# Optimization experiments

Hardware: AMD Instinct MI355X
Metric: run time of the kernel (lower is better)

The kernel has to match this reference:

```python
import jax, jax.numpy as jnp
import numpy as np

DMODEL = 512
NUM_HEADS = 8
DK = DMODEL // NUM_HEADS  # 64
CAUSAL = True


def setup_inputs() -> dict:
    key = jax.random.key(0)
    ks = jax.random.split(key, 11)
    B, S = 4, 2048
    s_in = 1.0 / np.sqrt(DMODEL)
    s_out = 1.0 / np.sqrt(NUM_HEADS * DK)
    return {
        "Q": jax.random.normal(ks[0], (B, S, DMODEL), jnp.float32),
        "K": jax.random.normal(ks[1], (B, S, DMODEL), jnp.float32),
        "V": jax.random.normal(ks[2], (B, S, DMODEL), jnp.float32),
        # torch nn.Linear weights stored as [in, out] (already transposed)
        "WQ_w": jax.random.uniform(ks[3], (DMODEL, DK), jnp.float32, -s_in, s_in),
        "WQ_b": jax.random.uniform(ks[4], (DK,), jnp.float32, -s_in, s_in),
        "WK_w": jax.random.uniform(ks[5], (DMODEL, DK), jnp.float32, -s_in, s_in),
        "WK_b": jax.random.uniform(ks[6], (DK,), jnp.float32, -s_in, s_in),
        "WV_w": jax.random.uniform(ks[7], (DMODEL, DK), jnp.float32, -s_in, s_in),
        "WV_b": jax.random.uniform(ks[8], (DK,), jnp.float32, -s_in, s_in),
        "Wo_w": jax.random.uniform(ks[9], (NUM_HEADS * DK, DMODEL), jnp.float32, -s_out, s_out),
        "Wo_b": jax.random.uniform(ks[10], (DMODEL,), jnp.float32, -s_out, s_out),
    }


def reference(Q, K, V, WQ_w, WQ_b, WK_w, WK_b, WV_w, WV_b, Wo_w, Wo_b):
    # Single shared projection to dk=64 (NOT per-head in the original module)
    q = Q @ WQ_w + WQ_b  # [B,S,dk]
    k = K @ WK_w + WK_b  # [B,S,dk]
    v = V @ WV_w + WV_b  # [B,S,dk]
    scores = jnp.einsum("bsd,btd->bst", q, k) / np.sqrt(DK).astype(np.float32)
    if CAUSAL:
        S = scores.shape[-1]
        causal = jnp.tril(jnp.ones((S, S), dtype=bool))  # True = keep
        scores = jnp.where(causal, scores, -jnp.inf)
    attn = jax.nn.softmax(scores, axis=-1)
    head_out = jnp.einsum("bst,btd->bsd", attn, v)  # [B,S,dk]
    # Every head is identical -> concat == tile num_heads copies
    concat = jnp.tile(head_out, (1, 1, NUM_HEADS))  # [B,S,num_heads*dk]
    return concat @ Wo_w + Wo_b  # [B,S,dmodel]
```

## Files before the change

### kernel.cpp

```cpp
#include <hip/hip_runtime.h>

#define DMODEL 512
#define DK 64
#define NH 8
#define SEQ 2048
#define BATCH 4
#define NROWS 8192
#define NEGBIG -1.0e30f
#define SPLITW 8
#define DKP 66
#define SHIFT2 8.656170245f
#define QSCALE 0.1803368801f

typedef _Float16 half_t;
typedef _Float16 half4 __attribute__((ext_vector_type(4)));
typedef _Float16 half8 __attribute__((ext_vector_type(8)));
typedef float floatx4 __attribute__((ext_vector_type(4)));

#ifdef __has_builtin
#  if __has_builtin(__builtin_amdgcn_exp2f)
#    define EXP2F(x) __builtin_amdgcn_exp2f(x)
#  endif
#  if __has_builtin(__builtin_amdgcn_cvt_pkrtz)
#    define HAVE_PKRTZ 1
#  endif
#  if __has_builtin(__builtin_amdgcn_mfma_f32_16x16x16f16)
#    define HAVE_MFMA16 1
#  endif
#endif
#ifndef EXP2F
#  define EXP2F(x) exp2f(x)
#endif
#ifndef HAVE_PKRTZ
#  define HAVE_PKRTZ 0
#endif
#ifndef HAVE_MFMA16
#  define HAVE_MFMA16 0
#endif

__device__ __forceinline__ half4 pk4(const float* p) {
#if HAVE_PKRTZ
    half4 r;
    auto lo = __builtin_amdgcn_cvt_pkrtz(p[0], p[1]);
    auto hi = __builtin_amdgcn_cvt_pkrtz(p[2], p[3]);
    __builtin_memcpy(&r, &lo, 4);
    __builtin_memcpy(reinterpret_cast<char*>(&r) + 4, &hi, 4);
    return r;
#else
    return (half4){(half_t)p[0], (half_t)p[1], (half_t)p[2], (half_t)p[3]};
#endif
}

__global__ __launch_bounds__(256) void prep_kernel(
    const float* __restrict__ WQ, const float* __restrict__ WK,
    const float* __restrict__ WV, const float* __restrict__ Wo,
    half_t* __restrict__ wtq, half_t* __restrict__ wtk, half_t* __restrict__ wtv,
    half_t* __restrict__ wo_tr)
{
    const int idx = blockIdx.x * 256 + threadIdx.x;
    const int k = idx >> 6;
    const int n = idx & 63;
    wtq[(size_t)n * DMODEL + k] = (half_t)WQ[idx];
    wtk[(size_t)n * DMODEL + k] = (half_t)WK[idx];
    wtv[(size_t)n * DMODEL + k] = (half_t)WV[idx];
    const int n2 = idx & 511;
    const int k2 = idx >> 9;
    float s = 0.f;
#pragma unroll
    for (int h = 0; h < NH; h++)
        s += Wo[((size_t)(h * DK + k2)) * DMODEL + n2];
    wo_tr[(size_t)n2 * DK + k2] = (half_t)s;
}

__global__ __launch_bounds__(128) void proj_kernel(
    const float* __restrict__ Q, const float* __restrict__ K, const float* __restrict__ V,
    const half_t* __restrict__ wtq, const half_t* __restrict__ wtk, const half_t* __restrict__ wtv,
    const float* __restrict__ bQ, const float* __restrict__ bK, const float* __restrict__ bV,
    half_t* __restrict__ qh, half_t* __restrict__ kh, half_t* __restrict__ vt)
{
    const int tens = blockIdx.y;
    const float* X  = (tens == 0) ? Q : (tens == 1) ? K : V;
    const half_t* wt = (tens == 0) ? wtq : (tens == 1) ? wtk : wtv;
    const float* bias = (tens == 0) ? bQ : (tens == 1) ? bK : bV;

    const int r0 = blockIdx.x * 16;
    const int tid = threadIdx.x;
    const int w = tid >> 6;
    const int lane = tid & 63;
    const int c = lane & 15;
    const int quad = lane >> 4;

    __shared__ floatx4 red[4][64];

    floatx4 acc[4] = {{0.f,0.f,0.f,0.f},{0.f,0.f,0.f,0.f},{0.f,0.f,0.f,0.f},{0.f,0.f,0.f,0.f}};

    const float* xrow = X + (size_t)(r0 + c) * DMODEL + quad * 8;
#pragma unroll 8
    for (int ks = w; ks < 16; ks += 2) {
        const float* xp = xrow + ks * 32;
        half8 a;
#pragma unroll
        for (int i = 0; i < 8; i++) a[i] = (half_t)xp[i];
#pragma unroll
        for (int nt = 0; nt < 4; nt++) {
            half8 bfr = *(const half8*)(wt + (size_t)(nt * 16 + c) * DMODEL + ks * 32 + quad * 8);
            acc[nt] = __builtin_amdgcn_mfma_f32_16x16x32_f16(a, bfr, acc[nt], 0, 0, 0);
        }
    }

    if (w == 1) {
#pragma unroll
        for (int nt = 0; nt < 4; nt++) red[nt][lane] = acc[nt];
    }
    __syncthreads();
    if (w == 1) return;

#pragma unroll
    for (int nt = 0; nt < 4; nt++) {
        const floatx4 r4 = red[nt][lane];
        const float bv = bias[nt * 16 + c];
#pragma unroll
        for (int r = 0; r < 4; r++) {
            const float val = acc[nt][r] + r4[r] + bv;
            const int row = r0 + quad * 4 + r;
            if (tens == 0) {
                qh[(size_t)row * DK + nt * 16 + c] = (half_t)(val * QSCALE);
            } else if (tens == 1) {
                kh[(size_t)row * DK + nt * 16 + c] = (half_t)val;
            } else {
                const int b  = row >> 11;
                const int s  = row & (SEQ - 1);
                const int kb = s >> 4;
                const int kk = s & 15;
                vt[(size_t)(b * 128 + kb) * 1024
                   + (size_t)c * 64 + (nt >> 1) * 32 + (kk >> 2) * 8 + (nt & 1) * 4 + (kk & 3)]
                    = (half_t)val;
            }
        }
    }
}

__global__ __launch_bounds__(512, 4) void attn_kernel(
    const half_t* __restrict__ qh, const half_t* __restrict__ kh,
    const half_t* __restrict__ vt, const half_t* __restrict__ wo_tr,
    const float* __restrict__ bo, float* __restrict__ out)
{
    const int bx = blockIdx.x;
    int b, qt;
    if (bx < 256) { qt = bx >> 1;            b = bx & 1; }
    else          { int k2 = bx - 256; qt = 127 - (k2 >> 1); b = 2 + (k2 & 1); }
    const int tid = threadIdx.x;
    const int w = tid >> 6;
    const int lane = tid & 63;
    const int c = lane & 15;
    const int quad = lane >> 4;

    __shared__ float sow[SPLITW][16][DKP];
    __shared__ float sl_s[SPLITW][16];
    __shared__ half_t of16[16][72];

    const half_t* qrow = qh + (size_t)(b * SEQ + qt * 16 + c) * DK + quad * 8;
    half8 qb0 = *(const half8*)(qrow);
    half8 qb1 = *(const half8*)(qrow + 32);

    float lp = 0.f;
    floatx4 o[4] = {{0.f,0.f,0.f,0.f},{0.f,0.f,0.f,0.f},{0.f,0.f,0.f,0.f},{0.f,0.f,0.f,0.f}};
    const floatx4 cinit = {-SHIFT2, -SHIFT2, -SHIFT2, -SHIFT2};

    const half_t* kbb = kh + (size_t)b * SEQ * DK;
    const half_t* vtb = vt + (size_t)b * 128 * 1024;

    int pb = w;
    half8 ka0, ka1, kb0, kb1;
    if (2 * pb <= qt) {
        const half_t* kr0 = kbb + (size_t)(2 * pb * 16 + c) * DK + quad * 8;
        ka0 = *(const half8*)(kr0);
        ka1 = *(const half8*)(kr0 + 32);
        const half_t* kr1 = kr0 + 16 * DK;
        kb0 = *(const half8*)(kr1);
        kb1 = *(const half8*)(kr1 + 32);
    }

    while (2 * pb <= qt) {
        const int t0 = 2 * pb, t1 = 2 * pb + 1;
        const half_t* vp0 = vtb + (size_t)t0 * 1024 + c * 64 + quad * 8;
        const half_t* vp1 = vtb + (size_t)t1 * 1024 + c * 64 + quad * 8;
        half8 va01 = *(const half8*)(vp0);
        half8 va23 = *(const half8*)(vp0 + 32);
        half8 vc01 = *(const half8*)(vp1);
        half8 vc23 = *(const half8*)(vp1 + 32);

        const int npb = pb + SPLITW;
        half8 nka0 = ka0, nka1 = ka1, nkb0 = kb0, nkb1 = kb1;
        if (2 * npb <= qt) {
            const half_t* nkr0 = kbb + (size_t)(2 * npb * 16 + c) * DK + quad * 8;
            nka0 = *(const half8*)(nkr0);
            nka1 = *(const half8*)(nkr0 + 32);
            const half_t* nkr1 = nkr0 + 16 * DK;
            nkb0 = *(const half8*)(nkr1);
            nkb1 = *(const half8*)(nkr1 + 32);
        }

        floatx4 sc0 = cinit;
        sc0 = __builtin_amdgcn_mfma_f32_16x16x32_f16(ka0, qb0, sc0, 0, 0, 0);
        sc0 = __builtin_amdgcn_mfma_f32_16x16x32_f16(ka1, qb1, sc0, 0, 0, 0);
        floatx4 sc1 = cinit;
        sc1 = __builtin_amdgcn_mfma_f32_16x16x32_f16(kb0, qb0, sc1, 0, 0, 0);
        sc1 = __builtin_amdgcn_mfma_f32_16x16x32_f16(kb1, qb1, sc1, 0, 0, 0);

        if (t0 == qt) {
#pragma unroll
            for (int r = 0; r < 4; r++) {
                if (quad * 4 + r > c) sc0[r] = NEGBIG;
                sc1[r] = NEGBIG;
            }
        } else if (t1 == qt) {
#pragma unroll
            for (int r = 0; r < 4; r++)
                if (quad * 4 + r > c) sc1[r] = NEGBIG;
        }

        float p0[4], p1[4];
#pragma unroll
        for (int r = 0; r < 4; r++) { p0[r] = EXP2F(sc0[r]); p1[r] = EXP2F(sc1[r]); }
        lp += (p0[0] + p0[1]) + (p0[2] + p0[3]) + ((p1[0] + p1[1]) + (p1[2] + p1[3]));

#if HAVE_MFMA16
        half4 pa = pk4(p0), pc = pk4(p1);
        half4 va0 = __builtin_shufflevector(va01, va01, 0, 1, 2, 3);
        half4 va1 = __builtin_shufflevector(va01, va01, 4, 5, 6, 7);
        half4 va2 = __builtin_shufflevector(va23, va23, 0, 1, 2, 3);
        half4 va3 = __builtin_shufflevector(va23, va23, 4, 5, 6, 7);
        half4 vc0 = __builtin_shufflevector(vc01, vc01, 0, 1, 2, 3);
        half4 vc1 = __builtin_shufflevector(vc01, vc01, 4, 5, 6, 7);
        half4 vc2 = __builtin_shufflevector(vc23, vc23, 0, 1, 2, 3);
        half4 vc3 = __builtin_shufflevector(vc23, vc23, 4, 5, 6, 7);
        o[0] = __builtin_amdgcn_mfma_f32_16x16x16f16(pa, va0, o[0], 0, 0, 0);
        o[1] = __builtin_amdgcn_mfma_f32_16x16x16f16(pa, va1, o[1], 0, 0, 0);
        o[2] = __builtin_amdgcn_mfma_f32_16x16x16f16(pa, va2, o[2], 0, 0, 0);
        o[3] = __builtin_amdgcn_mfma_f32_16x16x16f16(pa, va3, o[3], 0, 0, 0);
        o[0] = __builtin_amdgcn_mfma_f32_16x16x16f16(pc, vc0, o[0], 0, 0, 0);
        o[1] = __builtin_amdgcn_mfma_f32_16x16x16f16(pc, vc1, o[1], 0, 0, 0);
        o[2] = __builtin_amdgcn_mfma_f32_16x16x16f16(pc, vc2, o[2], 0, 0, 0);
        o[3] = __builtin_amdgcn_mfma_f32_16x16x16f16(pc, vc3, o[3], 0, 0, 0);
#else
        half8 pa8, pc8;
#pragma unroll
        for (int jj = 0; jj < 8; jj++) {
            const int src = (((quad * 2 + (jj >> 2)) & 3) * 16 + c);
            const float pj0 = __shfl(p0[jj & 3], src);
            const float pj1 = __shfl(p1[jj & 3], src);
            pa8[jj] = (quad < 2) ? (half_t)pj0 : (half_t)0.f;
            pc8[jj] = (quad < 2) ? (half_t)pj1 : (half_t)0.f;
        }
#pragma unroll
        for (int nt = 0; nt < 4; nt++) {
            const half_t* vb0 = vtb + (size_t)t0 * 1024 + c * 64 + (nt >> 1) * 32 + (quad & 1) * 16 + (nt & 1) * 4;
            half4 l0 = *(const half4*)(vb0);
            half4 h0 = *(const half4*)(vb0 + 8);
            half8 v80 = {l0[0], l0[1], l0[2], l0[3], h0[0], h0[1], h0[2], h0[3]};
            o[nt] = __builtin_amdgcn_mfma_f32_16x16x32_f16(pa8, v80, o[nt], 0, 0, 0);
            const half_t* vb1 = vtb + (size_t)t1 * 1024 + c * 64 + (nt >> 1) * 32 + (quad & 1) * 16 + (nt & 1) * 4;
            half4 l1 = *(const half4*)(vb1);
            half4 h1 = *(const half4*)(vb1 + 8);
            half8 v81 = {l1[0], l1[1], l1[2], l1[3], h1[0], h1[1], h1[2], h1[3]};
            o[nt] = __builtin_amdgcn_mfma_f32_16x16x32_f16(pc8, v81, o[nt], 0, 0, 0);
        }
#endif
        ka0 = nka0; ka1 = nka1; kb0 = nkb0; kb1 = nkb1; pb = npb;
    }

    lp += __shfl_xor(lp, 16);
    lp += __shfl_xor(lp, 32);

#pragma unroll
    for (int nt = 0; nt < 4; nt++)
#pragma unroll
        for (int r = 0; r < 4; r++)
            sow[w][quad * 4 + r][nt * 16 + c] = o[nt][r];
    if (quad == 0) sl_s[w][c] = lp;
    __syncthreads();

    {
        const int q = w * 2 + (lane >> 5);
        const int d0 = (lane & 31) * 2;
        float lstar = 0.f, acc0 = 0.f, acc1 = 0.f;
#pragma unroll
        for (int ww = 0; ww < SPLITW; ww++) {
            lstar += sl_s[ww][q];
            const float* sp = &sow[ww][q][d0];
            acc0 += sp[0];
            acc1 += sp[1];
        }
        const float linv = 1.f / lstar;
        of16[q][d0]     = (half_t)(acc0 * linv);
        of16[q][d0 + 1] = (half_t)(acc1 * linv);
    }
    __syncthreads();

    half8 a1 = *(const half8*)(&of16[c][quad * 8]);
    half8 a2 = *(const half8*)(&of16[c][32 + quad * 8]);
    const size_t orow = (size_t)(b * SEQ + qt * 16);
#pragma unroll
    for (int i = 0; i < 4; i++) {
        const int n = (w * 4 + i) * 16 + c;
        half8 b1 = *(const half8*)(wo_tr + (size_t)n * DK + quad * 8);
        half8 b2 = *(const half8*)(wo_tr + (size_t)n * DK + 32 + quad * 8);
        floatx4 oc = {0.f, 0.f, 0.f, 0.f};
        oc = __builtin_amdgcn_mfma_f32_16x16x32_f16(a1, b1, oc, 0, 0, 0);
        oc = __builtin_amdgcn_mfma_f32_16x16x32_f16(a2, b2, oc, 0, 0, 0);
        const float bv = bo[n];
#pragma unroll
        for (int r = 0; r < 4; r++)
            out[(orow + quad * 4 + r) * DMODEL + n] = oc[r] + bv;
    }
}

extern "C" void kernel_launch(void* const* d_in, const int* in_sizes, int n_in,
                              void* d_out, int out_size, void* d_ws, size_t ws_size,
                              hipStream_t stream) {
    const float* Q  = (const float*)d_in[0];
    const float* K  = (const float*)d_in[1];
    const float* V  = (const float*)d_in[2];
    const float* WQ = (const float*)d_in[3];
    const float* bQ = (const float*)d_in[4];
    const float* WK = (const float*)d_in[5];
    const float* bK = (const float*)d_in[6];
    const float* WV = (const float*)d_in[7];
    const float* bV = (const float*)d_in[8];
    const float* Wo = (const float*)d_in[9];
    const float* bo = (const float*)d_in[10];
    float* out = (float*)d_out;

    char* ws = (char*)d_ws;
    half_t* qh    = (half_t*)ws;
    half_t* kh    = (half_t*)(ws + (1u << 20));
    half_t* vt    = (half_t*)(ws + (2u << 20));
    half_t* wtq   = (half_t*)(ws + (3u << 20));
    half_t* wtk   = wtq + 32768;
    half_t* wtv   = wtk + 32768;
    half_t* wo_tr = wtv + 32768;

    prep_kernel<<<128, 256, 0, stream>>>(WQ, WK, WV, Wo, wtq, wtk, wtv, wo_tr);
    proj_kernel<<<dim3(512, 3), 128, 0, stream>>>(Q, K, V, wtq, wtk, wtv, bQ, bK, bV, qh, kh, vt);
    attn_kernel<<<512, 512, 0, stream>>>(qh, kh, vt, wo_tr, bo, out);
}
```

Before: 142.0 us.

## Fuse prep, projection and attention into one persistent kernel with grid barriers

Merges the three kernel launches (weight prep, QKV projection, attention plus output projection) into one 512-block kernel separated by software grid barriers built on atomic counters, with a memset to reset the counters. This removes the gaps and tail effects between launches. The barrier assumes all 512 blocks are resident at once, and it has a guard timeout that could silently break correctness if they are not. Packing three projection tiles per block into four 128-thread groups leaves one group idle during that phase.

```diff
diff --git a/kernel.cpp b/kernel.cpp
--- a/kernel.cpp
+++ b/kernel.cpp
@@ -5,7 +5,7 @@
 #define NH 8
 #define SEQ 2048
 #define BATCH 4
-#define NROWS 8192
+#define NBLOCKS 512
 #define NEGBIG -1.0e30f
 #define SPLITW 8
 #define DKP 66
@@ -51,268 +51,288 @@
 #endif
 }
 
-__global__ __launch_bounds__(256) void prep_kernel(
-    const float* __restrict__ WQ, const float* __restrict__ WK,
-    const float* __restrict__ WV, const float* __restrict__ Wo,
-    half_t* __restrict__ wtq, half_t* __restrict__ wtk, half_t* __restrict__ wtv,
-    half_t* __restrict__ wo_tr)
-{
-    const int idx = blockIdx.x * 256 + threadIdx.x;
-    const int k = idx >> 6;
-    const int n = idx & 63;
-    wtq[(size_t)n * DMODEL + k] = (half_t)WQ[idx];
-    wtk[(size_t)n * DMODEL + k] = (half_t)WK[idx];
-    wtv[(size_t)n * DMODEL + k] = (half_t)WV[idx];
-    const int n2 = idx & 511;
-    const int k2 = idx >> 9;
-    float s = 0.f;
-#pragma unroll
-    for (int h = 0; h < NH; h++)
-        s += Wo[((size_t)(h * DK + k2)) * DMODEL + n2];
-    wo_tr[(size_t)n2 * DK + k2] = (half_t)s;
-}
-
-__global__ __launch_bounds__(128) void proj_kernel(
-    const float* __restrict__ Q, const float* __restrict__ K, const float* __restrict__ V,
-    const half_t* __restrict__ wtq, const half_t* __restrict__ wtk, const half_t* __restrict__ wtv,
-    const float* __restrict__ bQ, const float* __restrict__ bK, const float* __restrict__ bV,
-    half_t* __restrict__ qh, half_t* __restrict__ kh, half_t* __restrict__ vt)
-{
-    const int tens = blockIdx.y;
-    const float* X  = (tens == 0) ? Q : (tens == 1) ? K : V;
-    const half_t* wt = (tens == 0) ? wtq : (tens == 1) ? wtk : wtv;
-    const float* bias = (tens == 0) ? bQ : (tens == 1) ? bK : bV;
-
-    const int r0 = blockIdx.x * 16;
-    const int tid = threadIdx.x;
-    const int w = tid >> 6;
-    const int lane = tid & 63;
-    const int c = lane & 15;
-    const int quad = lane >> 4;
-
-    __shared__ floatx4 red[4][64];
-
-    floatx4 acc[4] = {{0.f,0.f,0.f,0.f},{0.f,0.f,0.f,0.f},{0.f,0.f,0.f,0.f},{0.f,0.f,0.f,0.f}};
-
-    const float* xrow = X + (size_t)(r0 + c) * DMODEL + quad * 8;
-#pragma unroll 8
-    for (int ks = w; ks < 16; ks += 2) {
-        const float* xp = xrow + ks * 32;
-        half8 a;
-#pragma unroll
-        for (int i = 0; i < 8; i++) a[i] = (half_t)xp[i];
-#pragma unroll
-        for (int nt = 0; nt < 4; nt++) {
-            half8 bfr = *(const half8*)(wt + (size_t)(nt * 16 + c) * DMODEL + ks * 32 + quad * 8);
-            acc[nt] = __builtin_amdgcn_mfma_f32_16x16x32_f16(a, bfr, acc[nt], 0, 0, 0);
-        }
-    }
-
-    if (w == 1) {
-#pragma unroll
-        for (int nt = 0; nt < 4; nt++) red[nt][lane] = acc[nt];
+__device__ __forceinline__ void grid_barrier(unsigned* cnt) {
+    __syncthreads();
+    if (threadIdx.x == 0) {
+        __threadfence();
+        __hip_atomic_fetch_add(cnt, 1u, __ATOMIC_ACQ_REL, __HIP_MEMORY_SCOPE_AGENT);
+        int guard = 0;
+        while (__hip_atomic_load(cnt, __ATOMIC_ACQUIRE, __HIP_MEMORY_SCOPE_AGENT) < (unsigned)NBLOCKS) {
+            __builtin_amdgcn_s_sleep(8);
+            if (++guard > (1 << 18)) break;
+        }
     }
     __syncthreads();
-    if (w == 1) return;
-
-#pragma unroll
-    for (int nt = 0; nt < 4; nt++) {
-        const floatx4 r4 = red[nt][lane];
-        const float bv = bias[nt * 16 + c];
-#pragma unroll
-        for (int r = 0; r < 4; r++) {
-            const float val = acc[nt][r] + r4[r] + bv;
-            const int row = r0 + quad * 4 + r;
-            if (tens == 0) {
-                qh[(size_t)row * DK + nt * 16 + c] = (half_t)(val * QSCALE);
-            } else if (tens == 1) {
-                kh[(size_t)row * DK + nt * 16 + c] = (half_t)val;
-            } else {
-                const int b  = row >> 11;
-                const int s  = row & (SEQ - 1);
-                const int kb = s >> 4;
-                const int kk = s & 15;
-                vt[(size_t)(b * 128 + kb) * 1024
-                   + (size_t)c * 64 + (nt >> 1) * 32 + (kk >> 2) * 8 + (nt & 1) * 4 + (kk & 3)]
-                    = (half_t)val;
-            }
-        }
-    }
 }
 
-__global__ __launch_bounds__(512, 4) void attn_kernel(
-    const half_t* __restrict__ qh, const half_t* __restrict__ kh,
-    const half_t* __restrict__ vt, const half_t* __restrict__ wo_tr,
-    const float* __restrict__ bo, float* __restrict__ out)
+__global__ __launch_bounds__(512, 4) void fused_kernel(
+    const float* __restrict__ Q, const float* __restrict__ K, const float* __restrict__ V,
+    const float* __restrict__ WQ, const float* __restrict__ bQ,
+    const float* __restrict__ WK, const float* __restrict__ bK,
+    const float* __restrict__ WV, const float* __restrict__ bV,
+    const float* __restrict__ Wo, const float* __restrict__ bo,
+    float* __restrict__ out,
+    half_t* __restrict__ qh, half_t* __restrict__ kh, half_t* __restrict__ vt,
+    half_t* __restrict__ wtq, half_t* __restrict__ wtk, half_t* __restrict__ wtv,
+    half_t* __restrict__ wo_tr, unsigned* __restrict__ bar)
 {
     const int bx = blockIdx.x;
-    int b, qt;
-    if (bx < 256) { qt = bx >> 1;            b = bx & 1; }
-    else          { int k2 = bx - 256; qt = 127 - (k2 >> 1); b = 2 + (k2 & 1); }
     const int tid = threadIdx.x;
-    const int w = tid >> 6;
-    const int lane = tid & 63;
-    const int c = lane & 15;
-    const int quad = lane >> 4;
-
+
+    __shared__ floatx4 red[4][4][64];
     __shared__ float sow[SPLITW][16][DKP];
     __shared__ float sl_s[SPLITW][16];
     __shared__ half_t of16[16][72];
 
-    const half_t* qrow = qh + (size_t)(b * SEQ + qt * 16 + c) * DK + quad * 8;
-    half8 qb0 = *(const half8*)(qrow);
-    half8 qb1 = *(const half8*)(qrow + 32);
-
-    float lp = 0.f;
-    floatx4 o[4] = {{0.f,0.f,0.f,0.f},{0.f,0.f,0.f,0.f},{0.f,0.f,0.f,0.f},{0.f,0.f,0.f,0.f}};
-    const floatx4 cinit = {-SHIFT2, -SHIFT2, -SHIFT2, -SHIFT2};
-
-    const half_t* kbb = kh + (size_t)b * SEQ * DK;
-    const half_t* vtb = vt + (size_t)b * 128 * 1024;
-
-    int pb = w;
-    half8 ka0, ka1, kb0, kb1;
-    if (2 * pb <= qt) {
-        const half_t* kr0 = kbb + (size_t)(2 * pb * 16 + c) * DK + quad * 8;
-        ka0 = *(const half8*)(kr0);
-        ka1 = *(const half8*)(kr0 + 32);
-        const half_t* kr1 = kr0 + 16 * DK;
-        kb0 = *(const half8*)(kr1);
-        kb1 = *(const half8*)(kr1 + 32);
+    {
+        const int idx = bx * 512 + tid;
+        if (idx < 32768) {
+            const int k = idx >> 6;
+            const int n = idx & 63;
+            wtq[(size_t)n * DMODEL + k] = (half_t)WQ[idx];
+            wtk[(size_t)n * DMODEL + k] = (half_t)WK[idx];
+            wtv[(size_t)n * DMODEL + k] = (half_t)WV[idx];
+            const int n2 = idx & 511;
+            const int k2 = idx >> 9;
+            float s = 0.f;
+#pragma unroll
+            for (int h = 0; h < NH; h++)
+                s += Wo[((size_t)(h * DK + k2)) * DMODEL + n2];
+            wo_tr[(size_t)n2 * DK + k2] = (half_t)s;
+        }
     }
-
-    while (2 * pb <= qt) {
-        const int t0 = 2 * pb, t1 = 2 * pb + 1;
-        const half_t* vp0 = vtb + (size_t)t0 * 1024 + c * 64 + quad * 8;
-        const half_t* vp1 = vtb + (size_t)t1 * 1024 + c * 64 + quad * 8;
-        half8 va01 = *(const half8*)(vp0);
-        half8 va23 = *(const half8*)(vp0 + 32);
-        half8 vc01 = *(const half8*)(vp1);
-        half8 vc23 = *(const half8*)(vp1 + 32);
-
-        const int npb = pb + SPLITW;
-        half8 nka0 = ka0, nka1 = ka1, nkb0 = kb0, nkb1 = kb1;
-        if (2 * npb <= qt) {
-            const half_t* nkr0 = kbb + (size_t)(2 * npb * 16 + c) * DK + quad * 8;
-            nka0 = *(const half8*)(nkr0);
-            nka1 = *(const half8*)(nkr0 + 32);
-            const half_t* nkr1 = nkr0 + 16 * DK;
-            nkb0 = *(const half8*)(nkr1);
-            nkb1 = *(const half8*)(nkr1 + 32);
-        }
-
-        floatx4 sc0 = cinit;
-        sc0 = __builtin_amdgcn_mfma_f32_16x16x32_f16(ka0, qb0, sc0, 0, 0, 0);
-        sc0 = __builtin_amdgcn_mfma_f32_16x16x32_f16(ka1, qb1, sc0, 0, 0, 0);
-        floatx4 sc1 = cinit;
-        sc1 = __builtin_amdgcn_mfma_f32_16x16x32_f16(kb0, qb0, sc1, 0, 0, 0);
-        sc1 = __builtin_amdgcn_mfma_f32_16x16x32_f16(kb1, qb1, sc1, 0, 0, 0);
-
-        if (t0 == qt) {
-#pragma unroll
-            for (int r = 0; r < 4; r++) {
-                if (quad * 4 + r > c) sc0[r] = NEGBIG;
-                sc1[r] = NEGBIG;
-            }
-        } else if (t1 == qt) {
+    grid_barrier(&bar[0]);
+
+    {
+        const int wp = tid >> 7;
+        const int t2 = tid & 127;
+        const int w = t2 >> 6;
+        const int lane = t2 & 63;
+        const int c = lane & 15;
+        const int quad = lane >> 4;
+
+        int tens = 0, r0 = 0;
+        if (wp < 3) {
+            const int j = bx * 3 + wp;
+            tens = j >> 9;
+            r0 = (j & 511) * 16;
+        }
+        floatx4 acc[4] = {{0.f,0.f,0.f,0.f},{0.f,0.f,0.f,0.f},{0.f,0.f,0.f,0.f},{0.f,0.f,0.f,0.f}};
+        if (wp < 3) {
+            const float* __restrict__ X = (tens == 0) ? Q : (tens == 1) ? K : V;
+            const half_t* __restrict__ wt = (tens == 0) ? wtq : (tens == 1) ? wtk : wtv;
+            const float* xrow = X + (size_t)(r0 + c) * DMODEL + quad * 8;
+#pragma unroll 8
+            for (int ks = w; ks < 16; ks += 2) {
+                const float* xp = xrow + ks * 32;
+                half8 a;
+#pragma unroll
+                for (int i = 0; i < 8; i++) a[i] = (half_t)xp[i];
+#pragma unroll
+                for (int nt = 0; nt < 4; nt++) {
+                    half8 bfr = *(const half8*)(wt + (size_t)(nt * 16 + c) * DMODEL + ks * 32 + quad * 8);
+                    acc[nt] = __builtin_amdgcn_mfma_f32_16x16x32_f16(a, bfr, acc[nt], 0, 0, 0);
+                }
+            }
+            if (w == 1) {
+#pragma unroll
+                for (int nt = 0; nt < 4; nt++) red[wp][nt][lane] = acc[nt];
+            }
+        }
+        __syncthreads();
+        if (wp < 3 && w == 0) {
+            const float* __restrict__ bias = (tens == 0) ? bQ : (tens == 1) ? bK : bV;
+#pragma unroll
+            for (int nt = 0; nt < 4; nt++) {
+                const floatx4 r4 = red[wp][nt][lane];
+                const float bv = bias[nt * 16 + c];
+#pragma unroll
+                for (int r = 0; r < 4; r++) {
+                    const float val = acc[nt][r] + r4[r] + bv;
+                    const int row = r0 + quad * 4 + r;
+                    if (tens == 0) {
+                        qh[(size_t)row * DK + nt * 16 + c] = (half_t)(val * QSCALE);
+                    } else if (tens == 1) {
+                        kh[(size_t)row * DK + nt * 16 + c] = (half_t)val;
+                    } else {
+                        const int b  = row >> 11;
+                        const int s  = row & (SEQ - 1);
+                        const int kb = s >> 4;
+                        const int kk = s & 15;
+                        vt[(size_t)(b * 128 + kb) * 1024
+                           + (size_t)c * 64 + (nt >> 1) * 32 + (kk >> 2) * 8 + (nt & 1) * 4 + (kk & 3)]
+                            = (half_t)val;
+                    }
+                }
+            }
+        }
+    }
+    grid_barrier(&bar[1]);
+
+    {
+        int b, qt;
+        if (bx < 256) { qt = bx >> 1;                b = bx & 1; }
+        else          { const int k2 = bx - 256;     qt = 127 - (k2 >> 1); b = 2 + (k2 & 1); }
+        const int w = tid >> 6;
+        const int lane = tid & 63;
+        const int c = lane & 15;
+        const int quad = lane >> 4;
+
+        const half_t* qrow = qh + (size_t)(b * SEQ + qt * 16 + c) * DK + quad * 8;
+        half8 qb0 = *(const half8*)(qrow);
+        half8 qb1 = *(const half8*)(qrow + 32);
+
+        float lp = 0.f;
+        floatx4 o[4] = {{0.f,0.f,0.f,0.f},{0.f,0.f,0.f,0.f},{0.f,0.f,0.f,0.f},{0.f,0.f,0.f,0.f}};
+        const floatx4 cinit = {-SHIFT2, -SHIFT2, -SHIFT2, -SHIFT2};
+
+        const half_t* kbb = kh + (size_t)b * SEQ * DK;
+        const half_t* vtb = vt + (size_t)b * 128 * 1024;
+
+        int pb = w;
+        half8 ka0, ka1, kb0, kb1;
+        if (2 * pb <= qt) {
+            const half_t* kr0 = kbb + (size_t)(2 * pb * 16 + c) * DK + quad * 8;
+            ka0 = *(const half8*)(kr0);
+            ka1 = *(const half8*)(kr0 + 32);
+            const half_t* kr1 = kr0 + 16 * DK;
+            kb0 = *(const half8*)(kr1);
+            kb1 = *(const half8*)(kr1 + 32);
+        }
+
+        while (2 * pb <= qt) {
+            const int t0 = 2 * pb, t1 = 2 * pb + 1;
+            const half_t* vp0 = vtb + (size_t)t0 * 1024 + c * 64 + quad * 8;
+            const half_t* vp1 = vtb + (size_t)t1 * 1024 + c * 64 + quad * 8;
+            half8 va01 = *(const half8*)(vp0);
+            half8 va23 = *(const half8*)(vp0 + 32);
+            half8 vc01 = *(const half8*)(vp1);
+            half8 vc23 = *(const half8*)(vp1 + 32);
+
+            const int npb = pb + SPLITW;
+            half8 nka0 = ka0, nka1 = ka1, nkb0 = kb0, nkb1 = kb1;
+            if (2 * npb <= qt) {
+                const half_t* nkr0 = kbb + (size_t)(2 * npb * 16 + c) * DK + quad * 8;
+                nka0 = *(const half8*)(nkr0);
+                nka1 = *(const half8*)(nkr0 + 32);
+                const half_t* nkr1 = nkr0 + 16 * DK;
+                nkb0 = *(const half8*)(nkr1);
+                nkb1 = *(const half8*)(nkr1 + 32);
+            }
+
+            floatx4 sc0 = cinit;
+            sc0 = __builtin_amdgcn_mfma_f32_16x16x32_f16(ka0, qb0, sc0, 0, 0, 0);
+            sc0 = __builtin_amdgcn_mfma_f32_16x16x32_f16(ka1, qb1, sc0, 0, 0, 0);
+            floatx4 sc1 = cinit;
+            sc1 = __builtin_amdgcn_mfma_f32_16x16x32_f16(kb0, qb0, sc1, 0, 0, 0);
+            sc1 = __builtin_amdgcn_mfma_f32_16x16x32_f16(kb1, qb1, sc1, 0, 0, 0);
+
+            if (t0 == qt) {
+#pragma unroll
+                for (int r = 0; r < 4; r++) {
+                    if (quad * 4 + r > c) sc0[r] = NEGBIG;
+                    sc1[r] = NEGBIG;
+                }
+            } else if (t1 == qt) {
+#pragma unroll
+                for (int r = 0; r < 4; r++)
+                    if (quad * 4 + r > c) sc1[r] = NEGBIG;
+            }
+
+            float p0[4], p1[4];
+#pragma unroll
+            for (int r = 0; r < 4; r++) { p0[r] = EXP2F(sc0[r]); p1[r] = EXP2F(sc1[r]); }
+            lp += (p0[0] + p0[1]) + (p0[2] + p0[3]) + ((p1[0] + p1[1]) + (p1[2] + p1[3]));
+
+#if HAVE_MFMA16
+            half4 pa = pk4(p0), pc = pk4(p1);
+            half4 va0 = __builtin_shufflevector(va01, va01, 0, 1, 2, 3);
+            half4 va1 = __builtin_shufflevector(va01, va01, 4, 5, 6, 7);
+            half4 va2 = __builtin_shufflevector(va23, va23, 0, 1, 2, 3);
+            half4 va3 = __builtin_shufflevector(va23, va23, 4, 5, 6, 7);
+            half4 vc0 = __builtin_shufflevector(vc01, vc01, 0, 1, 2, 3);
+            half4 vc1 = __builtin_shufflevector(vc01, vc01, 4, 5, 6, 7);
+            half4 vc2 = __builtin_shufflevector(vc23, vc23, 0, 1, 2, 3);
+            half4 vc3 = __builtin_shufflevector(vc23, vc23, 4, 5, 6, 7);
+            o[0] = __builtin_amdgcn_mfma_f32_16x16x16f16(pa, va0, o[0], 0, 0, 0);
+            o[1] = __builtin_amdgcn_mfma_f32_16x16x16f16(pa, va1, o[1], 0, 0, 0);
+            o[2] = __builtin_amdgcn_mfma_f32_16x16x16f16(pa, va2, o[2], 0, 0, 0);
+            o[3] = __builtin_amdgcn_mfma_f32_16x16x16f16(pa, va3, o[3], 0, 0, 0);
+            o[0] = __builtin_amdgcn_mfma_f32_16x16x16f16(pc, vc0, o[0], 0, 0, 0);
+            o[1] = __builtin_amdgcn_mfma_f32_16x16x16f16(pc, vc1, o[1], 0, 0, 0);
+            o[2] = __builtin_amdgcn_mfma_f32_16x16x16f16(pc, vc2, o[2], 0, 0, 0);
+            o[3] = __builtin_amdgcn_mfma_f32_16x16x16f16(pc, vc3, o[3], 0, 0, 0);
+#else
+            half8 pa8, pc8;
+#pragma unroll
+            for (int jj = 0; jj < 8; jj++) {
+                const int src = (((quad * 2 + (jj >> 2)) & 3) * 16 + c);
+                const float pj0 = __shfl(p0[jj & 3], src);
+                const float pj1 = __shfl(p1[jj & 3], src);
+                pa8[jj] = (quad < 2) ? (half_t)pj0 : (half_t)0.f;
+                pc8[jj] = (quad < 2) ? (half_t)pj1 : (half_t)0.f;
+            }
+#pragma unroll
+            for (int nt = 0; nt < 4; nt++) {
+                const half_t* vb0 = vtb + (size_t)t0 * 1024 + c * 64 + (nt >> 1) * 32 + (quad & 1) * 16 + (nt & 1) * 4;
+                half4 l0 = *(const half4*)(vb0);
+                half4 h0 = *(const half4*)(vb0 + 8);
+                half8 v80 = {l0[0], l0[1], l0[2], l0[3], h0[0], h0[1], h0[2], h0[3]};
+                o[nt] = __builtin_amdgcn_mfma_f32_16x16x32_f16(pa8, v80, o[nt], 0, 0, 0);
+                const half_t* vb1 = vtb + (size_t)t1 * 1024 + c * 64 + (nt >> 1) * 32 + (quad & 1) * 16 + (nt & 1) * 4;
+                half4 l1 = *(const half4*)(vb1);
+                half4 h1 = *(const half4*)(vb1 + 8);
+                half8 v81 = {l1[0], l1[1], l1[2], l1[3], h1[0], h1[1], h1[2], h1[3]};
+                o[nt] = __builtin_amdgcn_mfma_f32_16x16x32_f16(pc8, v81, o[nt], 0, 0, 0);
+            }
+#endif
+            ka0 = nka0; ka1 = nka1; kb0 = nkb0; kb1 = nkb1; pb = npb;
+        }
+
+        lp += __shfl_xor(lp, 16);
+        lp += __shfl_xor(lp, 32);
+
+#pragma unroll
+        for (int nt = 0; nt < 4; nt++)
 #pragma unroll
             for (int r = 0; r < 4; r++)
-                if (quad * 4 + r > c) sc1[r] = NEGBIG;
-        }
-
-        float p0[4], p1[4];
-#pragma unroll
-        for (int r = 0; r < 4; r++) { p0[r] = EXP2F(sc0[r]); p1[r] = EXP2F(sc1[r]); }
-        lp += (p0[0] + p0[1]) + (p0[2] + p0[3]) + ((p1[0] + p1[1]) + (p1[2] + p1[3]));
-
-#if HAVE_MFMA16
-        half4 pa = pk4(p0), pc = pk4(p1);
-        half4 va0 = __builtin_shufflevector(va01, va01, 0, 1, 2, 3);
-        half4 va1 = __builtin_shufflevector(va01, va01, 4, 5, 6, 7);
-        half4 va2 = __builtin_shufflevector(va23, va23, 0, 1, 2, 3);
-        half4 va3 = __builtin_shufflevector(va23, va23, 4, 5, 6, 7);
-        half4 vc0 = __builtin_shufflevector(vc01, vc01, 0, 1, 2, 3);
-        half4 vc1 = __builtin_shufflevector(vc01, vc01, 4, 5, 6, 7);
-        half4 vc2 = __builtin_shufflevector(vc23, vc23, 0, 1, 2, 3);
-        half4 vc3 = __builtin_shufflevector(vc23, vc23, 4, 5, 6, 7);
-        o[0] = __builtin_amdgcn_mfma_f32_16x16x16f16(pa, va0, o[0], 0, 0, 0);
-        o[1] = __builtin_amdgcn_mfma_f32_16x16x16f16(pa, va1, o[1], 0, 0, 0);
-        o[2] = __builtin_amdgcn_mfma_f32_16x16x16f16(pa, va2, o[2], 0, 0, 0);
-        o[3] = __builtin_amdgcn_mfma_f32_16x16x16f16(pa, va3, o[3], 0, 0, 0);
-        o[0] = __builtin_amdgcn_mfma_f32_16x16x16f16(pc, vc0, o[0], 0, 0, 0);
-        o[1] = __builtin_amdgcn_mfma_f32_16x16x16f16(pc, vc1, o[1], 0, 0, 0);
-        o[2] = __builtin_amdgcn_mfma_f32_16x16x16f16(pc, vc2, o[2], 0, 0, 0);
-        o[3] = __builtin_amdgcn_mfma_f32_16x16x16f16(pc, vc3, o[3], 0, 0, 0);
-#else
-        half8 pa8, pc8;
-#pragma unroll
-        for (int jj = 0; jj < 8; jj++) {
-            const int src = (((quad * 2 + (jj >> 2)) & 3) * 16 + c);
-            const float pj0 = __shfl(p0[jj & 3], src);
-            const float pj1 = __shfl(p1[jj & 3], src);
-            pa8[jj] = (quad < 2) ? (half_t)pj0 : (half_t)0.f;
-            pc8[jj] = (quad < 2) ? (half_t)pj1 : (half_t)0.f;
-        }
-#pragma unroll
-        for (int nt = 0; nt < 4; nt++) {
-            const half_t* vb0 = vtb + (size_t)t0 * 1024 + c * 64 + (nt >> 1) * 32 + (quad & 1) * 16 + (nt & 1) * 4;
-            half4 l0 = *(const half4*)(vb0);
-            half4 h0 = *(const half4*)(vb0 + 8);
-            half8 v80 = {l0[0], l0[1], l0[2], l0[3], h0[0], h0[1], h0[2], h0[3]};
-            o[nt] = __builtin_amdgcn_mfma_f32_16x16x32_f16(pa8, v80, o[nt], 0, 0, 0);
-            const half_t* vb1 = vtb + (size_t)t1 * 1024 + c * 64 + (nt >> 1) * 32 + (quad & 1) * 16 + (nt & 1) * 4;
-            half4 l1 = *(const half4*)(vb1);
-            half4 h1 = *(const half4*)(vb1 + 8);
-            half8 v81 = {l1[0], l1[1], l1[2], l1[3], h1[0], h1[1], h1[2], h1[3]};
-            o[nt] = __builtin_amdgcn_mfma_f32_16x16x32_f16(pc8, v81, o[nt], 0, 0, 0);
-        }
-#endif
-        ka0 = nka0; ka1 = nka1; kb0 = nkb0; kb1 = nkb1; pb = npb;
-    }
-
-    lp += __shfl_xor(lp, 16);
-    lp += __shfl_xor(lp, 32);
-
-#pragma unroll
-    for (int nt = 0; nt < 4; nt++)
-#pragma unroll
-        for (int r = 0; r < 4; r++)
-            sow[w][quad * 4 + r][nt * 16 + c] = o[nt][r];
-    if (quad == 0) sl_s[w][c] = lp;
-    __syncthreads();
-
-    {
-        const int q = w * 2 + (lane >> 5);
-        const int d0 = (lane & 31) * 2;
-        float lstar = 0.f, acc0 = 0.f, acc1 = 0.f;
-#pragma unroll
-        for (int ww = 0; ww < SPLITW; ww++) {
-            lstar += sl_s[ww][q];
-            const float* sp = &sow[ww][q][d0];
-            acc0 += sp[0];
-            acc1 += sp[1];
-        }
-        const float linv = 1.f / lstar;
-        of16[q][d0]     = (half_t)(acc0 * linv);
-        of16[q][d0 + 1] = (half_t)(acc1 * linv);
-    }
-    __syncthreads();
-
-    half8 a1 = *(const half8*)(&of16[c][quad * 8]);
-    half8 a2 = *(const half8*)(&of16[c][32 + quad * 8]);
-    const size_t orow = (size_t)(b * SEQ + qt * 16);
-#pragma unroll
-    for (int i = 0; i < 4; i++) {
-        const int n = (w * 4 + i) * 16 + c;
-        half8 b1 = *(const half8*)(wo_tr + (size_t)n * DK + quad * 8);
-        half8 b2 = *(const half8*)(wo_tr + (size_t)n * DK + 32 + quad * 8);
-        floatx4 oc = {0.f, 0.f, 0.f, 0.f};
-        oc = __builtin_amdgcn_mfma_f32_16x16x32_f16(a1, b1, oc, 0, 0, 0);
-        oc = __builtin_amdgcn_mfma_f32_16x16x32_f16(a2, b2, oc, 0, 0, 0);
-        const float bv = bo[n];
-#pragma unroll
-        for (int r = 0; r < 4; r++)
-            out[(orow + quad * 4 + r) * DMODEL + n] = oc[r] + bv;
+                sow[w][quad * 4 + r][nt * 16 + c] = o[nt][r];
+        if (quad == 0) sl_s[w][c] = lp;
+        __syncthreads();
+
+        {
+            const int q = w * 2 + (lane >> 5);
+            const int d0 = (lane & 31) * 2;
+            float lstar = 0.f, acc0 = 0.f, acc1 = 0.f;
+#pragma unroll
+            for (int ww = 0; ww < SPLITW; ww++) {
+                lstar += sl_s[ww][q];
+                const float* sp = &sow[ww][q][d0];
+                acc0 += sp[0];
+                acc1 += sp[1];
+            }
+            const float linv = 1.f / lstar;
+            of16[q][d0]     = (half_t)(acc0 * linv);
+            of16[q][d0 + 1] = (half_t)(acc1 * linv);
+        }
+        __syncthreads();
+
+        half8 a1 = *(const half8*)(&of16[c][quad * 8]);
+        half8 a2 = *(const half8*)(&of16[c][32 + quad * 8]);
+        const size_t orow = (size_t)(b * SEQ + qt * 16);
+#pragma unroll
+        for (int i = 0; i < 4; i++) {
+            const int n = (w * 4 + i) * 16 + c;
+            half8 b1 = *(const half8*)(wo_tr + (size_t)n * DK + quad * 8);
+            half8 b2 = *(const half8*)(wo_tr + (size_t)n * DK + 32 + quad * 8);
+            floatx4 oc = {0.f, 0.f, 0.f, 0.f};
+            oc = __builtin_amdgcn_mfma_f32_16x16x32_f16(a1, b1, oc, 0, 0, 0);
+            oc = __builtin_amdgcn_mfma_f32_16x16x32_f16(a2, b2, oc, 0, 0, 0);
+            const float bv = bo[n];
+#pragma unroll
+            for (int r = 0; r < 4; r++)
+                out[(orow + quad * 4 + r) * DMODEL + n] = oc[r] + bv;
+        }
     }
 }
 
@@ -340,8 +360,10 @@
     half_t* wtk   = wtq + 32768;
     half_t* wtv   = wtk + 32768;
     half_t* wo_tr = wtv + 32768;
-
-    prep_kernel<<<128, 256, 0, stream>>>(WQ, WK, WV, Wo, wtq, wtk, wtv, wo_tr);
-    proj_kernel<<<dim3(512, 3), 128, 0, stream>>>(Q, K, V, wtq, wtk, wtv, bQ, bK, bV, qh, kh, vt);
-    attn_kernel<<<512, 512, 0, stream>>>(qh, kh, vt, wo_tr, bo, out);
+    unsigned* bar = (unsigned*)(ws + (4u << 20));
+
+    hipMemsetAsync(bar, 0, 128, stream);
+    fused_kernel<<<NBLOCKS, 512, 0, stream>>>(
+        Q, K, V, WQ, bQ, WK, bK, WV, bV, Wo, bo, out,
+        qh, kh, vt, wtq, wtk, wtv, wo_tr, bar);
 }
```

New measurement: 268.1 us. 1.89x slower.
